# Optimization experiments

Hardware: AMD Instinct MI355X
Metric: run time of the kernel (lower is better)

The kernel has to match this reference:

```python
import jax, jax.numpy as jnp
import numpy as np

H = 64      # hidden_num
IN = 8      # input_num
P = 8192    # number of POIs
N = 8192    # graph nodes
SCALING = 2.0
NEG_INF = -9e15
ALPHA = 0.2  # leaky relu slope in GAT


def gru_cell(x, h, Wih, Whh, bih, bhh):
    # torch.nn.GRUCell math
    gi = x @ Wih.T + bih
    gh = h @ Whh.T + bhh
    ir, iz, inn = jnp.split(gi, 3, axis=1)
    hr, hz, hn = jnp.split(gh, 3, axis=1)
    r = jax.nn.sigmoid(ir + hr)
    z = jax.nn.sigmoid(iz + hz)
    n = jnp.tanh(inn + r * hn)
    return (1.0 - z) * n + z * h


def gat_layer(h, adj, W, a):
    # pyGAT GraphAttentionLayer (eval mode, no dropout)
    Wh = h @ W                      # [N, F']
    F = W.shape[1]
    e1 = Wh @ a[:F]                 # [N, 1]
    e2 = Wh @ a[F:]                 # [N, 1]
    e = jax.nn.leaky_relu(e1 + e2.T, negative_slope=ALPHA)  # [N, N]
    e = jnp.where(adj > 0, e, NEG_INF)
    attn = jax.nn.softmax(e, axis=1)
    return attn @ Wh                # [N, F']


def gat_forward(nodes, adj, gatW, gatA, gatWout, gatAout):
    # 4 heads, concat, then output layer; log_softmax at the end
    heads = [jax.nn.elu(gat_layer(nodes, adj, gatW[k], gatA[k])) for k in range(gatW.shape[0])]
    x1 = jnp.concatenate(heads, axis=1)                      # [N, 16]
    out = jax.nn.elu(gat_layer(x1, adj, gatWout, gatAout))   # [N, 2]
    return jax.nn.log_softmax(out, axis=1)


def setup_inputs() -> dict:
    key = jax.random.key(0)
    ks = jax.random.split(key, 24)
    s = 0.1  # keep params small so exp() terms stay in range
    inp = {
        "x": jax.random.normal(ks[0], (1, IN), jnp.float32),
        "user": jax.random.uniform(ks[1], (1, 1), jnp.float32),
        "nextHid": jax.random.normal(ks[2], (1, H), jnp.float32),
        "periodHid": jax.random.normal(ks[3], (1, H), jnp.float32),
        "qhh": jnp.ones((H, H), jnp.float32),
        "aH": jnp.zeros((H, H), jnp.float32),
        "poi_loc": jax.random.normal(ks[4], (P, 2), jnp.float32),
        "poi_dist": jax.random.uniform(ks[5], (P,), jnp.float32),
        "nodes": jax.random.normal(ks[6], (N, 4), jnp.float32),
        "pre": 0,
    }
    # sparse-ish random adjacency (avg degree ~32) with self loops, dense [N,N] as in pyGAT
    mask = (jax.random.uniform(ks[7], (N, N)) < (32.0 / N)).astype(jnp.float32)
    inp["edges"] = jnp.maximum(mask, jnp.eye(N, dtype=jnp.float32))
    # learned parameters
    inp["w"] = jax.random.normal(ks[8], (1, 1), jnp.float32) * s
    inp["Wih1"] = jax.random.normal(ks[9], (3 * H, IN), jnp.float32) * s
    inp["Whh1"] = jax.random.normal(ks[10], (3 * H, H), jnp.float32) * s
    inp["bih1"] = jax.random.normal(ks[11], (3 * H,), jnp.float32) * s
    inp["bhh1"] = jax.random.normal(ks[12], (3 * H,), jnp.float32) * s
    inp["Wih3"] = jax.random.normal(ks[13], (3 * H, IN + 1), jnp.float32) * s
    inp["Whh3"] = jax.random.normal(ks[14], (3 * H, H), jnp.float32) * s
    inp["bih3"] = jax.random.normal(ks[15], (3 * H,), jnp.float32) * s
    inp["bhh3"] = jax.random.normal(ks[16], (3 * H,), jnp.float32) * s
    inp["gatW"] = jax.random.normal(ks[17], (4, 4, 4), jnp.float32) * s
    inp["gatA"] = jax.random.normal(ks[18], (4, 8, 1), jnp.float32) * s
    inp["gatWout"] = jax.random.normal(ks[19], (16, 2), jnp.float32) * s
    inp["gatAout"] = jax.random.normal(ks[20], (4, 1), jnp.float32) * s
    return inp


def reference(x, user, nextHid, periodHid, qhh, aH, poi_loc, poi_dist, nodes, edges, pre,
              w, Wih1, Whh1, bih1, bhh1, Wih3, Whh3, bih3, bhh3,
              gatW, gatA, gatWout, gatAout):
    # --- sequence GRU step (lastTime is None branch -> GRUCell1) ---
    nextHid = gru_cell(x, nextHid, Wih1, Whh1, bih1, bhh1)          # [1, H]
    h = nextHid[0]                                                   # [H]

    # --- distance-weighted POI attention, fully vectorized ---
    d = jnp.exp(-poi_dist / SCALING)                                 # [P]
    # qLis_p = (nextHid^T) @ w @ eLi_p  -> outer(h, loc_p) * w
    E = jnp.exp(w[0, 0] * h[None, :, None] * poi_loc[:, None, :] * d[:, None, None])  # [P, H, 2]
    allwe = E.sum(axis=0)                                            # [H, 2]
    cL = jnp.einsum('phe,pe->h', E / allwe, poi_loc)[:, None]        # [H, 1]

    # --- periodicity GRU + attention ---
    xin = jnp.concatenate([user, x], axis=1)                         # [1, IN+1]
    periodHid = gru_cell(xin, periodHid, Wih3, Whh3, bih3, bhh3)     # [1, H]
    qhi = jnp.exp(nextHid.T @ periodHid)                             # [H, H]
    qhh = qhh + qhi
    aH = aH + qhi / qhh
    cP = aH @ periodHid.T                                            # [H, 1]

    # --- GAT over the POI graph ---
    outGAT = gat_forward(nodes, edges, gatW, gatA, gatWout, gatAout) # [N, 2]

    # --- scoring: anw_p = max_j (g_p . loc_p) * mL_j ---
    mL = jnp.concatenate([nextHid, cL.T, cP.T], axis=1)              # [1, 3H]
    g = jax.lax.dynamic_slice_in_dim(outGAT, pre, P, axis=0)         # [P, 2]
    s = jnp.einsum('pk,pk->p', g, poi_loc)                           # [P]
    anw_logits = jnp.max(s[:, None] * mL, axis=1)                    # [P]
    anw = jax.nn.softmax(anw_logits)
    value, index = jax.lax.top_k(anw, 5)
    return (nextHid, periodHid, qhh, aH, index)
```

## Files before the change

kernel.cpp:

```cpp
#include <hip/hip_runtime.h>
#include <math.h>

#define H64 64
#define IN8 8
#define PNUM 8192
#define NNUM 8192
#define ALPHA_LR 0.2f
#define MAXDEG 128
#define SEGCAP 96
#define FRONTB 81
#define TB_GAT 1024
#define TB_CL  1024
#define TB_RED 1025
#define TB_N   1057

typedef float f32x4 __attribute__((ext_vector_type(4)));

constexpr int WS_NH = 0;
constexpr int WS_PH = 64;
constexpr int WS_CP = 128;
constexpr int WS_MAXML = 256;
constexpr int WS_MINML = 257;
constexpr int WS_PART = 320;
constexpr int WS_NF2 = 262656;
constexpr int WS_LOGITS = 295424;
constexpr int WS_DEG = 303616;
constexpr int WS_NBR = 311808;
constexpr int WS_TPART = 574016;
constexpr int WS_CNTA = 574400;
constexpr int WS_CNTB = 574401;

__device__ __forceinline__ float sigm_(float x) { return 1.0f / (1.0f + expf(-x)); }
__device__ __forceinline__ float elu_(float x) { return x > 0.0f ? x : expm1f(x); }

__global__ __launch_bounds__(256) void k_main(
    const float* __restrict__ x, const float* __restrict__ user,
    const float* __restrict__ nh0, const float* __restrict__ ph0,
    const float* __restrict__ qhh_in, const float* __restrict__ aH_in,
    const float* __restrict__ loc, const float* __restrict__ dist,
    const float* __restrict__ wscal,
    const float* __restrict__ Wih1, const float* __restrict__ Whh1,
    const float* __restrict__ bih1, const float* __restrict__ bhh1,
    const float* __restrict__ Wih3, const float* __restrict__ Whh3,
    const float* __restrict__ bih3, const float* __restrict__ bhh3,
    const float* __restrict__ nodes, const float* __restrict__ gatW,
    const float* __restrict__ gatA, const float* __restrict__ Wout,
    const float* __restrict__ Aout, const float* __restrict__ edges,
    float* __restrict__ ws, float* __restrict__ out,
    int* __restrict__ deg, int* __restrict__ nbr) {
    __shared__ float snh[64], sph[64];
    __shared__ float sl[256], sde[128];
    __shared__ int s_seg[4][SEGCAP];
    __shared__ int s_cnt[4];
    __shared__ int s_all[4 * SEGCAP];
    __shared__ float s_head[4][5];
    const int b = blockIdx.x, tid = threadIdx.x;

    if (b < FRONTB) {
        if (tid < 64) {
            int t = tid;
            float gir = bih1[t], giz = bih1[H64 + t], gin = bih1[2 * H64 + t];
            for (int c = 0; c < IN8; ++c) {
                float xv = x[c];
                gir += xv * Wih1[t * IN8 + c];
                giz += xv * Wih1[(H64 + t) * IN8 + c];
                gin += xv * Wih1[(2 * H64 + t) * IN8 + c];
            }
            float ghr = bhh1[t], ghz = bhh1[H64 + t], ghn = bhh1[2 * H64 + t];
            for (int c = 0; c < H64; ++c) {
                float hv = nh0[c];
                ghr += hv * Whh1[t * H64 + c];
                ghz += hv * Whh1[(H64 + t) * H64 + c];
                ghn += hv * Whh1[(2 * H64 + t) * H64 + c];
            }
            float r = sigm_(gir + ghr), z = sigm_(giz + ghz);
            float n = tanhf(gin + r * ghn);
            snh[t] = (1.0f - z) * n + z * nh0[t];
        } else if (tid < 128) {
            int t = tid - 64;
            const int INC = IN8 + 1;
            float gir = bih3[t], giz = bih3[H64 + t], gin = bih3[2 * H64 + t];
            for (int c = 0; c < INC; ++c) {
                float xv = (c == 0) ? user[0] : x[c - 1];
                gir += xv * Wih3[t * INC + c];
                giz += xv * Wih3[(H64 + t) * INC + c];
                gin += xv * Wih3[(2 * H64 + t) * INC + c];
            }
            float ghr = bhh3[t], ghz = bhh3[H64 + t], ghn = bhh3[2 * H64 + t];
            for (int c = 0; c < H64; ++c) {
                float hv = ph0[c];
                ghr += hv * Whh3[t * H64 + c];
                ghz += hv * Whh3[(H64 + t) * H64 + c];
                ghn += hv * Whh3[(2 * H64 + t) * H64 + c];
            }
            float r = sigm_(gir + ghr), z = sigm_(giz + ghz);
            float n = tanhf(gin + r * ghn);
            sph[t] = (1.0f - z) * n + z * ph0[t];
        }
        __syncthreads();

        if (b < 16) {
            int w = tid >> 6, j = tid & 63;
            int i = b * 4 + w;
            float qhi = expf(snh[i] * sph[j]);
            float qn = qhh_in[i * H64 + j] + qhi;
            float an = aH_in[i * H64 + j] + qhi / qn;
            out[128 + i * H64 + j] = qn;
            out[128 + H64 * H64 + i * H64 + j] = an;
            float v = an * sph[j];
            for (int off = 32; off >= 1; off >>= 1) v += __shfl_xor(v, off);
            if (j == 0) ws[WS_CP + i] = v;
        } else if (b < 80) {
            int p0 = (b - 16) * 128;
            sl[tid] = loc[p0 * 2 + tid];
            if (tid < 128) sde[tid] = expf(-dist[p0 + tid] * 0.5f);
            __syncthreads();
            int h = tid & 63, sub = tid >> 6;
            float a = wscal[0] * snh[h];
            float4 s = make_float4(0.f, 0.f, 0.f, 0.f);
            for (int pp = sub * 32; pp < sub * 32 + 32; ++pp) {
                float l0 = sl[2 * pp], l1 = sl[2 * pp + 1], dd = sde[pp];
                float E0 = expf(a * l0 * dd);
                float E1 = expf(a * l1 * dd);
                s.x += E0; s.y += E0 * l0; s.z += E1; s.w += E1 * l1;
            }
            ((float4*)(ws + WS_PART))[((b - 16) * 4 + sub) * 64 + h] = s;
        } else {
            if (tid == 0) { ((int*)(ws + WS_CNTA))[0] = 0; ((int*)(ws + WS_CNTB))[0] = 0; }
            if (tid < 64) { ws[WS_NH + tid] = snh[tid]; out[tid] = snh[tid]; }
            else if (tid < 128) { int t = tid - 64; ws[WS_PH + t] = sph[t]; out[64 + t] = sph[t]; }
        }
        return;
    }

    const int wave = tid >> 6, lane = tid & 63;
    const int row = b - FRONTB;
    const f32x4* erow = (const f32x4*)(edges + (size_t)row * NNUM);
    const unsigned long long lmask = (1ull << lane) - 1ull;

    float wk[4][4], a1v[4], a2v[4];
#pragma unroll
    for (int r = 0; r < 4; ++r)
#pragma unroll
        for (int f = 0; f < 4; ++f) wk[r][f] = gatW[wave * 16 + r * 4 + f];
#pragma unroll
    for (int f = 0; f < 4; ++f) { a1v[f] = gatA[wave * 8 + f]; a2v[f] = gatA[wave * 8 + 4 + f]; }

    float4 ndr = *(const float4*)(nodes + (size_t)row * 4);
    float e1k;
    {
        float w0 = ndr.x * wk[0][0] + ndr.y * wk[1][0] + ndr.z * wk[2][0] + ndr.w * wk[3][0];
        float w1 = ndr.x * wk[0][1] + ndr.y * wk[1][1] + ndr.z * wk[2][1] + ndr.w * wk[3][1];
        float w2 = ndr.x * wk[0][2] + ndr.y * wk[1][2] + ndr.z * wk[2][2] + ndr.w * wk[3][2];
        float w3 = ndr.x * wk[0][3] + ndr.y * wk[1][3] + ndr.z * wk[2][3] + ndr.w * wk[3][3];
        e1k = w0 * a1v[0] + w1 * a1v[1] + w2 * a1v[2] + w3 * a1v[3];
    }

    f32x4 bchunk[8];
#pragma unroll
    for (int u = 0; u < 8; ++u)
        bchunk[u] = __builtin_nontemporal_load(&erow[wave * 512 + u * 64 + lane]);
    int base = 0;
#pragma unroll
    for (int u = 0; u < 8; ++u) {
        f32x4 cv = bchunk[u];
        float mx01 = fmaxf(cv[0], cv[1]);
        float mx23 = fmaxf(cv[2], cv[3]);
        bool any = fmaxf(mx01, mx23) > 0.0f;
        unsigned long long am = __ballot(any);
        if (am == 0ull) continue;
        int jb = wave * 2048 + u * 256 + lane * 4;
#pragma unroll
        for (int c = 0; c < 4; ++c) {
            bool hit = cv[c] > 0.0f;
            unsigned long long mask = __ballot(hit);
            if (hit) {
                int pos = base + __popcll(mask & lmask);
                if (pos < SEGCAP) s_seg[wave][pos] = jb + c;
            }
            base += __popcll(mask);
        }
    }
    if (lane == 0) s_cnt[wave] = base < SEGCAP ? base : SEGCAP;
    __syncthreads();

    int c0 = s_cnt[0], c1 = s_cnt[1], c2 = s_cnt[2], c3 = s_cnt[3];
    int offw = (wave > 0 ? c0 : 0) + (wave > 1 ? c1 : 0) + (wave > 2 ? c2 : 0);
    int cw = s_cnt[wave];
    for (int s = lane; s < cw; s += 64) s_all[offw + s] = s_seg[wave][s];
    __syncthreads();

    int d = c0 + c1 + c2 + c3;
    int dcl = d < MAXDEG ? d : MAXDEG;
    if (tid == 0) deg[row] = dcl;
    for (int s = tid; s < dcl; s += 256) nbr[row * MAXDEG + s] = s_all[s];

    float den = 0.0f, a0 = 0.0f, a1 = 0.0f, a2 = 0.0f, a3 = 0.0f;
    for (int s = lane; s < d; s += 64) {
        int j = s_all[s];
        float4 nd = *(const float4*)(nodes + (size_t)j * 4);
        float w0 = nd.x * wk[0][0] + nd.y * wk[1][0] + nd.z * wk[2][0] + nd.w * wk[3][0];
        float w1 = nd.x * wk[0][1] + nd.y * wk[1][1] + nd.z * wk[2][1] + nd.w * wk[3][1];
        float w2 = nd.x * wk[0][2] + nd.y * wk[1][2] + nd.z * wk[2][2] + nd.w * wk[3][2];
        float w3 = nd.x * wk[0][3] + nd.y * wk[1][3] + nd.z * wk[2][3] + nd.w * wk[3][3];
        float e2 = w0 * a2v[0] + w1 * a2v[1] + w2 * a2v[2] + w3 * a2v[3];
        float e = e1k + e2;
        float lr = e >= 0.0f ? e : ALPHA_LR * e;
        float p = __expf(lr);
        den += p;
        a0 += p * w0; a1 += p * w1; a2 += p * w2; a3 += p * w3;
    }
    for (int off = 1; off < 64; off <<= 1) {
        den += __shfl_xor(den, off);
        a0 += __shfl_xor(a0, off);
        a1 += __shfl_xor(a1, off);
        a2 += __shfl_xor(a2, off);
        a3 += __shfl_xor(a3, off);
    }
    if (lane == 0) {
        s_head[wave][0] = den;
        s_head[wave][1] = a0; s_head[wave][2] = a1;
        s_head[wave][3] = a2; s_head[wave][4] = a3;
    }
    __syncthreads();
    if (tid == 0) {
        float x1v[16];
#pragma unroll
        for (int k = 0; k < 4; ++k) {
            float dk = s_head[k][0];
#pragma unroll
            for (int f = 0; f < 4; ++f) x1v[k * 4 + f] = elu_(s_head[k][1 + f] / dk);
        }
        float v0 = 0, v1 = 0;
#pragma unroll
        for (int c = 0; c < 16; ++c) {
            v0 += x1v[c] * Wout[c * 2 + 0];
            v1 += x1v[c] * Wout[c * 2 + 1];
        }
        float ee1 = v0 * Aout[0] + v1 * Aout[1];
        float ee2 = v0 * Aout[2] + v1 * Aout[3];
        float4* nf2 = (float4*)(ws + WS_NF2 + row * 4);
        *nf2 = make_float4(ee1, ee2, v0, v1);
    }
}

__global__ __launch_bounds__(256) void k_tail(const float* __restrict__ loc,
                                              const int* __restrict__ pre_p,
                                              float* __restrict__ ws,
                                              const int* __restrict__ deg,
                                              const int* __restrict__ nbr,
                                              float* __restrict__ out) {
    __shared__ float red[4][64][4];
    __shared__ unsigned long long sk[256 * 5];
    __shared__ int slast;
    const int b = blockIdx.x, tid = threadIdx.x;
    const int wave = tid >> 6, lane = tid & 63;
    float* logits = ws + WS_LOGITS;
    int* cntA = (int*)(ws + WS_CNTA);
    int* cntB = (int*)(ws + WS_CNTB);
    unsigned long long* part = (unsigned long long*)(ws + WS_TPART);

    if (b < TB_GAT) {
        int start = pre_p[0];
        if (start < 0) start = 0;
        if (start > NNUM - PNUM) start = NNUM - PNUM;
        const float4* nf2 = (const float4*)(ws + WS_NF2);
#pragma unroll
        for (int rr = 0; rr < 2; ++rr) {
            int row = b * 8 + wave * 2 + rr;
            float e1r = ws[WS_NF2 + row * 4];
            int d = deg[row];
            const int* nrow = nbr + row * MAXDEG;
            float den = 0, a0 = 0, a1 = 0;
            for (int s = lane; s < d; s += 64) {
                int j = nrow[s];
                float4 nf = nf2[j];
                float e = e1r + nf.y;
                float lr = e >= 0.0f ? e : ALPHA_LR * e;
                float p = __expf(lr);
                den += p; a0 += p * nf.z; a1 += p * nf.w;
            }
            for (int off = 1; off < 64; off <<= 1) {
                den += __shfl_xor(den, off);
                a0 += __shfl_xor(a0, off);
                a1 += __shfl_xor(a1, off);
            }
            if (lane == 0) {
                float o0 = elu_(a0 / den), o1 = elu_(a1 / den);
                float mm = fmaxf(o0, o1);
                float lse = mm + logf(expf(o0 - mm) + expf(o1 - mm));
                float l0 = o0 - lse, l1 = o1 - lse;
                int p = row - start;
                if (p >= 0 && p < PNUM) {
                    float sval = l0 * loc[p * 2 + 0] + l1 * loc[p * 2 + 1];
                    __hip_atomic_store(&logits[p], sval, __ATOMIC_RELAXED, __HIP_MEMORY_SCOPE_AGENT);
                }
            }
        }
        asm volatile("s_waitcnt vmcnt(0)" ::: "memory");
        __syncthreads();
        if (tid == 0) __hip_atomic_fetch_add(cntA, 1, __ATOMIC_RELAXED, __HIP_MEMORY_SCOPE_AGENT);
        return;
    }

    if (b == TB_CL) {
        int h = tid & 63, g = tid >> 6;
        const float4* partc = (const float4*)(ws + WS_PART);
        float4 s = make_float4(0.f, 0.f, 0.f, 0.f);
        for (int seg = g; seg < 256; seg += 4) {
            float4 p = partc[seg * 64 + h];
            s.x += p.x; s.y += p.y; s.z += p.z; s.w += p.w;
        }
        red[g][h][0] = s.x; red[g][h][1] = s.y; red[g][h][2] = s.z; red[g][h][3] = s.w;
        __syncthreads();
        if (tid < 64) {
            float sd0 = 0, sn0 = 0, sd1 = 0, sn1 = 0;
            for (int g2 = 0; g2 < 4; ++g2) {
                sd0 += red[g2][tid][0]; sn0 += red[g2][tid][1];
                sd1 += red[g2][tid][2]; sn1 += red[g2][tid][3];
            }
            float cl = sn0 / sd0 + sn1 / sd1;
            float av = ws[WS_NH + tid], cv = ws[WS_CP + tid];
            float mx = fmaxf(fmaxf(av, cl), cv);
            float mn = fminf(fminf(av, cl), cv);
            for (int off = 32; off >= 1; off >>= 1) {
                mx = fmaxf(mx, __shfl_xor(mx, off));
                mn = fminf(mn, __shfl_xor(mn, off));
            }
            if (tid == 0) {
                __hip_atomic_store(&ws[WS_MAXML], mx, __ATOMIC_RELAXED, __HIP_MEMORY_SCOPE_AGENT);
                __hip_atomic_store(&ws[WS_MINML], mn, __ATOMIC_RELAXED, __HIP_MEMORY_SCOPE_AGENT);
            }
        }
        asm volatile("s_waitcnt vmcnt(0)" ::: "memory");
        __syncthreads();
        if (tid == 0) __hip_atomic_fetch_add(cntA, 1, __ATOMIC_RELAXED, __HIP_MEMORY_SCOPE_AGENT);
        return;
    }

    const int rid = b - TB_RED;
    if (tid == 0) {
        while (__hip_atomic_load(cntA, __ATOMIC_RELAXED, __HIP_MEMORY_SCOPE_AGENT) < TB_GAT + 1)
            __builtin_amdgcn_s_sleep(2);
    }
    __syncthreads();
    float mx = __hip_atomic_load(&ws[WS_MAXML], __ATOMIC_RELAXED, __HIP_MEMORY_SCOPE_AGENT);
    float mn = __hip_atomic_load(&ws[WS_MINML], __ATOMIC_RELAXED, __HIP_MEMORY_SCOPE_AGENT);
    int p = rid * 256 + tid;
    float s = __hip_atomic_load(&logits[p], __ATOMIC_RELAXED, __HIP_MEMORY_SCOPE_AGENT);
    float val = s > 0.0f ? s * mx : s * mn;
    unsigned u = __float_as_uint(val);
    u = (u & 0x80000000u) ? ~u : (u | 0x80000000u);
    unsigned long long key = ((unsigned long long)u << 32) | (unsigned)(PNUM - 1 - p);
    sk[tid * 5] = key;
#pragma unroll
    for (int q = 1; q < 5; ++q) sk[tid * 5 + q] = 0ull;
    __syncthreads();
    for (int stride = 128; stride >= 1; stride >>= 1) {
        if (tid < stride) {
            unsigned long long r[5];
            int ia = 0, ib = 0;
            int ab = tid * 5, bb = (tid + stride) * 5;
#pragma unroll
            for (int q = 0; q < 5; ++q) {
                unsigned long long av = sk[ab + ia], bv = sk[bb + ib];
                if (av >= bv) { r[q] = av; ++ia; } else { r[q] = bv; ++ib; }
            }
#pragma unroll
            for (int q = 0; q < 5; ++q) sk[ab + q] = r[q];
        }
        __syncthreads();
    }
    if (tid < 5)
        __hip_atomic_store(&part[rid * 5 + tid], sk[tid], __ATOMIC_RELAXED, __HIP_MEMORY_SCOPE_AGENT);
    if (tid == 0) {
        asm volatile("s_waitcnt vmcnt(0)" ::: "memory");
        int old = __hip_atomic_fetch_add(cntB, 1, __ATOMIC_RELAXED, __HIP_MEMORY_SCOPE_AGENT);
        slast = (old == 31) ? 1 : 0;
    }
    __syncthreads();
    if (!slast) return;
    unsigned long long k2 = (tid < 160)
        ? __hip_atomic_load(&part[tid], __ATOMIC_RELAXED, __HIP_MEMORY_SCOPE_AGENT) : 0ull;
    __syncthreads();
    sk[tid * 5] = k2;
#pragma unroll
    for (int q = 1; q < 5; ++q) sk[tid * 5 + q] = 0ull;
    __syncthreads();
    for (int stride = 128; stride >= 1; stride >>= 1) {
        if (tid < stride) {
            unsigned long long r[5];
            int ia = 0, ib = 0;
            int ab = tid * 5, bb = (tid + stride) * 5;
#pragma unroll
            for (int q = 0; q < 5; ++q) {
                unsigned long long av = sk[ab + ia], bv = sk[bb + ib];
                if (av >= bv) { r[q] = av; ++ia; } else { r[q] = bv; ++ib; }
            }
#pragma unroll
            for (int q = 0; q < 5; ++q) sk[ab + q] = r[q];
        }
        __syncthreads();
    }
    if (tid == 0) {
#pragma unroll
        for (int q = 0; q < 5; ++q)
            out[8320 + q] = (float)(PNUM - 1 - (int)(sk[q] & 0xFFFFFFFFull));
    }
}

extern "C" void kernel_launch(void* const* d_in, const int* in_sizes, int n_in,
                              void* d_out, int out_size, void* d_ws, size_t ws_size,
                              hipStream_t stream) {
    const float* x        = (const float*)d_in[0];
    const float* user     = (const float*)d_in[1];
    const float* nextHid  = (const float*)d_in[2];
    const float* periodHid= (const float*)d_in[3];
    const float* qhh      = (const float*)d_in[4];
    const float* aH       = (const float*)d_in[5];
    const float* poi_loc  = (const float*)d_in[6];
    const float* poi_dist = (const float*)d_in[7];
    const float* nodes    = (const float*)d_in[8];
    const int*   pre      = (const int*)d_in[9];
    const float* edges    = (const float*)d_in[10];
    const float* w        = (const float*)d_in[11];
    const float* Wih1     = (const float*)d_in[12];
    const float* Whh1     = (const float*)d_in[13];
    const float* bih1     = (const float*)d_in[14];
    const float* bhh1     = (const float*)d_in[15];
    const float* Wih3     = (const float*)d_in[16];
    const float* Whh3     = (const float*)d_in[17];
    const float* bih3     = (const float*)d_in[18];
    const float* bhh3     = (const float*)d_in[19];
    const float* gatW     = (const float*)d_in[20];
    const float* gatA     = (const float*)d_in[21];
    const float* gatWout  = (const float*)d_in[22];
    const float* gatAout  = (const float*)d_in[23];
    float* out = (float*)d_out;
    float* ws  = (float*)d_ws;
    int* deg = (int*)(ws + WS_DEG);
    int* nbr = (int*)(ws + WS_NBR);

    hipLaunchKernelGGL(k_main, dim3(FRONTB + NNUM), dim3(256), 0, stream,
                       x, user, nextHid, periodHid, qhh, aH, poi_loc, poi_dist, w,
                       Wih1, Whh1, bih1, bhh1, Wih3, Whh3, bih3, bhh3,
                       nodes, gatW, gatA, gatWout, gatAout, edges, ws, out, deg, nbr);
    hipLaunchKernelGGL(k_tail, dim3(TB_N), dim3(256), 0, stream, poi_loc, pre, ws, deg, nbr, out);
}
```

Measured before the change: 86.90 us.

## Split GAT tail into per-segment completion counters and one row per wave

Replaces the single global completion counter with one counter per 256-row segment plus separate counters for the cL block and the final merge. Each top-k reduction block now waits only for its own segment and the cL result, not for every GAT block. The GAT output stage also doubles its block count so each wave handles one row, which adds parallelism at the cost of more block launches and atomics. The `pre` offset handling is dropped because the row start always clamps to 0 when N equals P.

```diff
diff --git a/kernel.cpp b/kernel.cpp
--- a/kernel.cpp
+++ b/kernel.cpp
@@ -9,10 +9,10 @@
 #define MAXDEG 128
 #define SEGCAP 96
 #define FRONTB 81
-#define TB_GAT 1024
-#define TB_CL  1024
-#define TB_RED 1025
-#define TB_N   1057
+#define TB_GAT 2048
+#define TB_CL  2048
+#define TB_RED 2049
+#define TB_N   2081
 
 typedef float f32x4 __attribute__((ext_vector_type(4)));
 
@@ -27,8 +27,7 @@
 constexpr int WS_DEG = 303616;
 constexpr int WS_NBR = 311808;
 constexpr int WS_TPART = 574016;
-constexpr int WS_CNTA = 574400;
-constexpr int WS_CNTB = 574401;
+constexpr int WS_CNTS = 574400;
 
 __device__ __forceinline__ float sigm_(float x) { return 1.0f / (1.0f + expf(-x)); }
 __device__ __forceinline__ float elu_(float x) { return x > 0.0f ? x : expm1f(x); }
@@ -126,7 +125,7 @@
             }
             ((float4*)(ws + WS_PART))[((b - 16) * 4 + sub) * 64 + h] = s;
         } else {
-            if (tid == 0) { ((int*)(ws + WS_CNTA))[0] = 0; ((int*)(ws + WS_CNTB))[0] = 0; }
+            if (tid < 34) ((int*)(ws + WS_CNTS))[tid] = 0;
             if (tid < 64) { ws[WS_NH + tid] = snh[tid]; out[tid] = snh[tid]; }
             else if (tid < 128) { int t = tid - 64; ws[WS_PH + t] = sph[t]; out[64 + t] = sph[t]; }
         }
@@ -256,50 +255,40 @@
     const int b = blockIdx.x, tid = threadIdx.x;
     const int wave = tid >> 6, lane = tid & 63;
     float* logits = ws + WS_LOGITS;
-    int* cntA = (int*)(ws + WS_CNTA);
-    int* cntB = (int*)(ws + WS_CNTB);
+    int* cnts = (int*)(ws + WS_CNTS);
     unsigned long long* part = (unsigned long long*)(ws + WS_TPART);
 
     if (b < TB_GAT) {
-        int start = pre_p[0];
-        if (start < 0) start = 0;
-        if (start > NNUM - PNUM) start = NNUM - PNUM;
+        const int row = b * 4 + wave;
         const float4* nf2 = (const float4*)(ws + WS_NF2);
-#pragma unroll
-        for (int rr = 0; rr < 2; ++rr) {
-            int row = b * 8 + wave * 2 + rr;
-            float e1r = ws[WS_NF2 + row * 4];
-            int d = deg[row];
-            const int* nrow = nbr + row * MAXDEG;
-            float den = 0, a0 = 0, a1 = 0;
-            for (int s = lane; s < d; s += 64) {
-                int j = nrow[s];
-                float4 nf = nf2[j];
-                float e = e1r + nf.y;
-                float lr = e >= 0.0f ? e : ALPHA_LR * e;
-                float p = __expf(lr);
-                den += p; a0 += p * nf.z; a1 += p * nf.w;
-            }
-            for (int off = 1; off < 64; off <<= 1) {
-                den += __shfl_xor(den, off);
-                a0 += __shfl_xor(a0, off);
-                a1 += __shfl_xor(a1, off);
-            }
-            if (lane == 0) {
-                float o0 = elu_(a0 / den), o1 = elu_(a1 / den);
-                float mm = fmaxf(o0, o1);
-                float lse = mm + logf(expf(o0 - mm) + expf(o1 - mm));
-                float l0 = o0 - lse, l1 = o1 - lse;
-                int p = row - start;
-                if (p >= 0 && p < PNUM) {
-                    float sval = l0 * loc[p * 2 + 0] + l1 * loc[p * 2 + 1];
-                    __hip_atomic_store(&logits[p], sval, __ATOMIC_RELAXED, __HIP_MEMORY_SCOPE_AGENT);
-                }
-            }
+        float e1r = ws[WS_NF2 + row * 4];
+        int d = deg[row];
+        const int* nrow = nbr + row * MAXDEG;
+        float den = 0, a0 = 0, a1 = 0;
+        for (int s = lane; s < d; s += 64) {
+            int j = nrow[s];
+            float4 nf = nf2[j];
+            float e = e1r + nf.y;
+            float lr = e >= 0.0f ? e : ALPHA_LR * e;
+            float p = __expf(lr);
+            den += p; a0 += p * nf.z; a1 += p * nf.w;
+        }
+        for (int off = 1; off < 64; off <<= 1) {
+            den += __shfl_xor(den, off);
+            a0 += __shfl_xor(a0, off);
+            a1 += __shfl_xor(a1, off);
+        }
+        if (lane == 0) {
+            float o0 = elu_(a0 / den), o1 = elu_(a1 / den);
+            float mm = fmaxf(o0, o1);
+            float lse = mm + logf(expf(o0 - mm) + expf(o1 - mm));
+            float l0 = o0 - lse, l1 = o1 - lse;
+            float sval = l0 * loc[row * 2 + 0] + l1 * loc[row * 2 + 1];
+            __hip_atomic_store(&logits[row], sval, __ATOMIC_RELAXED, __HIP_MEMORY_SCOPE_AGENT);
         }
         asm volatile("s_waitcnt vmcnt(0)" ::: "memory");
         __syncthreads();
-        if (tid == 0) __hip_atomic_fetch_add(cntA, 1, __ATOMIC_RELAXED, __HIP_MEMORY_SCOPE_AGENT);
+        if (tid == 0) __hip_atomic_fetch_add(&cnts[b >> 6], 1, __ATOMIC_RELAXED, __HIP_MEMORY_SCOPE_AGENT);
         return;
     }
 
@@ -334,13 +323,14 @@
         }
         asm volatile("s_waitcnt vmcnt(0)" ::: "memory");
         __syncthreads();
-        if (tid == 0) __hip_atomic_fetch_add(cntA, 1, __ATOMIC_RELAXED, __HIP_MEMORY_SCOPE_AGENT);
+        if (tid == 0) __hip_atomic_fetch_add(&cnts[32], 1, __ATOMIC_RELAXED, __HIP_MEMORY_SCOPE_AGENT);
         return;
     }
 
     const int rid = b - TB_RED;
     if (tid == 0) {
-        while (__hip_atomic_load(cntA, __ATOMIC_RELAXED, __HIP_MEMORY_SCOPE_AGENT) < TB_GAT + 1)
+        while (__hip_atomic_load(&cnts[rid], __ATOMIC_RELAXED, __HIP_MEMORY_SCOPE_AGENT) < 64 ||
+               __hip_atomic_load(&cnts[32], __ATOMIC_RELAXED, __HIP_MEMORY_SCOPE_AGENT) < 1)
             __builtin_amdgcn_s_sleep(2);
     }
     __syncthreads();
@@ -375,7 +365,7 @@
         __hip_atomic_store(&part[rid * 5 + tid], sk[tid], __ATOMIC_RELAXED, __HIP_MEMORY_SCOPE_AGENT);
     if (tid == 0) {
         asm volatile("s_waitcnt vmcnt(0)" ::: "memory");
-        int old = __hip_atomic_fetch_add(cntB, 1, __ATOMIC_RELAXED, __HIP_MEMORY_SCOPE_AGENT);
+        int old = __hip_atomic_fetch_add(&cnts[33], 1, __ATOMIC_RELAXED, __HIP_MEMORY_SCOPE_AGENT);
         slast = (old == 31) ? 1 : 0;
     }
     __syncthreads();
```

Result: slower. 90.20 us (+3.8%).
